# Performance work log

Hardware: AMD Instinct MI355X
Metric: run time of the kernel (lower is better)

Reference implementation:

```python
import jax, jax.numpy as jnp
import numpy as np

NC = 4        # num_components
HEADS = 24
DH = 64
D = HEADS * DH  # 1536
EPS = 1e-8


def setup_inputs() -> dict:
    key = jax.random.key(0)
    ks = jax.random.split(key, 7)
    btc, S, E = 4, 4096, 154
    w = lambda k: jax.random.normal(k, (D, D), jnp.float32) * 0.02
    return {
        "hidden_states": jax.random.normal(ks[0], (btc, S, D), jnp.float32),
        "encoder_hidden_states": jax.random.normal(ks[1], (btc, E, D), jnp.float32),
        "temperature": jnp.ones((1,), jnp.float32),
        "Wq": w(ks[2]),
        "Wk": w(ks[3]),
        "Wv": w(ks[4]),
        "Wo": w(ks[5]),
        "bo": jnp.zeros((D,), jnp.float32),
        "pad_length": 154,
    }


def reference(hidden_states, encoder_hidden_states, temperature, Wq, Wk, Wv, Wo, bo, pad_length):
    btc, S, d = hidden_states.shape          # batch*components, latent seq, hidden
    E = encoder_hidden_states.shape[1]       # encoder seq (== pad_length)
    b = btc // NC
    scale = DH ** -0.5
    residual = hidden_states

    def heads(x, L):  # [btc, L, D] -> [btc, H, L, dh]
        return x.reshape(btc, L, HEADS, DH).transpose(0, 2, 1, 3)

    q = heads(hidden_states @ Wq.T, S)
    k = heads(encoder_hidden_states @ Wk.T, E)
    v = heads(encoder_hidden_states @ Wv.T, E)

    # pad tokens are zeros projected through the same k/v weights (no bias -> zeros)
    pad_h = jnp.zeros((btc, pad_length, d), hidden_states.dtype)
    k_pad = heads(pad_h @ Wk.T, pad_length)
    v_pad = heads(pad_h @ Wv.T, pad_length)

    scores = jnp.einsum('bhsd,bhed->bhse', q, k) / (temperature[0] + EPS)
    scores_pad = jnp.einsum('bhsd,bhpd->bhsp', q, k_pad) * scale

    # cross-component softmax over dim 0
    scores = scores.reshape(NC, b, HEADS, S, E)
    scores_pad = scores_pad.reshape(NC, b, HEADS, S, pad_length)
    w = jax.nn.softmax(scores, axis=0)
    w_pad = jax.nn.softmax(scores_pad, axis=0) * (NC / pad_length) * (1.0 - w)

    weights = jnp.concatenate(
        [w.reshape(btc, HEADS, S, E), w_pad.reshape(btc, HEADS, S, pad_length)],
        axis=-1)                              # [btc, H, S, E+pad]
    v_cat = jnp.concatenate([v, v_pad], axis=2)  # [btc, H, E+pad, dh]

    out = jnp.einsum('bhse,bhed->bhsd', weights, v_cat)
    out = out.transpose(0, 2, 1, 3).reshape(btc, S, d)
    out = out @ Wo.T + bo
    return out + residual
```

## Files before the change

### kernel.cpp

```cpp
#include <hip/hip_runtime.h>

typedef __attribute__((ext_vector_type(8))) short short8;
typedef __attribute__((ext_vector_type(4))) float f32x4;
typedef __attribute__((ext_vector_type(4))) unsigned short us4;
typedef __attribute__((ext_vector_type(4))) float float4v;

#define GLB_PTR(p) ((const __attribute__((address_space(1))) void*)(p))
#define LDS_PTR(p) ((__attribute__((address_space(3))) void*)(p))

__device__ __forceinline__ unsigned short f2bf(float f) {
  unsigned int u = __float_as_uint(f);
  u += 0x7FFF + ((u >> 16) & 1);
  return (unsigned short)(u >> 16);
}

__global__ void cvt_kernel(const float* __restrict__ in, unsigned short* __restrict__ out, int n4) {
  int i = blockIdx.x * blockDim.x + threadIdx.x;
  int stride = gridDim.x * blockDim.x;
  for (; i < n4; i += stride) {
    float4v v = *(const float4v*)(in + (size_t)i * 4);
    us4 o;
    o[0] = f2bf(v[0]); o[1] = f2bf(v[1]); o[2] = f2bf(v[2]); o[3] = f2bf(v[3]);
    *(us4*)(out + (size_t)i * 4) = o;
  }
}

__global__ void cvt4_kernel(const float* __restrict__ w0, const float* __restrict__ w1,
                            const float* __restrict__ w2, const float* __restrict__ w3,
                            unsigned short* __restrict__ o0, unsigned short* __restrict__ o1,
                            unsigned short* __restrict__ o2, unsigned short* __restrict__ o3,
                            int n4) {
  const float* in = blockIdx.y == 0 ? w0 : blockIdx.y == 1 ? w1 : blockIdx.y == 2 ? w2 : w3;
  unsigned short* out = blockIdx.y == 0 ? o0 : blockIdx.y == 1 ? o1 : blockIdx.y == 2 ? o2 : o3;
  int i = blockIdx.x * blockDim.x + threadIdx.x;
  int stride = gridDim.x * blockDim.x;
  for (; i < n4; i += stride) {
    float4v v = *(const float4v*)(in + (size_t)i * 4);
    us4 o;
    o[0] = f2bf(v[0]); o[1] = f2bf(v[1]); o[2] = f2bf(v[2]); o[3] = f2bf(v[3]);
    *(us4*)(out + (size_t)i * 4) = o;
  }
}

template<int MODE>
__global__ __launch_bounds__(256, 2) void gemm_big(
    const unsigned short* __restrict__ A,
    const unsigned short* __restrict__ B,
    unsigned short* __restrict__ Cb,
    float* __restrict__ Cf,
    const float* __restrict__ bias,
    const float* __restrict__ resid) {
  constexpr int K = 1536, N = 1536, BK = 32, NKT = K / BK;
  __shared__ unsigned short As[3][256 * 32];
  __shared__ unsigned short Bs[3][128 * 32];

  const int bid = blockIdx.x;
  const int xcd = bid & 7, idx = bid >> 3;
  const int m0 = (xcd * 8 + idx / 12) * 256;
  const int n0 = (idx % 12) * 128;

  const int t = threadIdx.x;
  const int w = t >> 6, l = t & 63, lr = l & 15, lg = l >> 4;
  const int wr = w >> 1, wc = w & 1;
  const int ga = lg ^ (lr & 3);

  const int srow = t >> 2;
  const int sg = (t & 3) ^ (srow & 3);
  const unsigned short* aSrc = A + (size_t)(m0 + srow) * K + sg * 8;
  const unsigned short* bSrc = B + (size_t)(n0 + srow) * K + sg * 8;

  f32x4 acc[8][4] = {};

  auto stage = [&](int buf, int kt) {
    const int k0 = kt * BK;
    unsigned short* AsW = &As[buf][0] + w * 512;
    unsigned short* BsW = &Bs[buf][0] + w * 512;
#pragma unroll
    for (int i = 0; i < 4; ++i)
      __builtin_amdgcn_global_load_lds(GLB_PTR(aSrc + (size_t)(i * 64) * K + k0), LDS_PTR(AsW + i * 2048), 16, 0, 0);
#pragma unroll
    for (int i = 0; i < 2; ++i)
      __builtin_amdgcn_global_load_lds(GLB_PTR(bSrc + (size_t)(i * 64) * K + k0), LDS_PTR(BsW + i * 2048), 16, 0, 0);
  };

  auto loadfrags = [&](int buf, short8* af, short8* bfv) {
    const unsigned short* Asb = &As[buf][0];
    const unsigned short* Bsb = &Bs[buf][0];
#pragma unroll
    for (int i = 0; i < 8; ++i)
      af[i] = *(const short8*)(Asb + (wr * 128 + i * 16 + lr) * 32 + ga * 8);
#pragma unroll
    for (int j = 0; j < 4; ++j)
      bfv[j] = *(const short8*)(Bsb + (wc * 64 + j * 16 + lr) * 32 + ga * 8);
  };

  auto mfma_all = [&](short8* af, short8* bfv) {
#pragma unroll
    for (int i = 0; i < 8; ++i)
#pragma unroll
      for (int j = 0; j < 4; ++j)
        acc[i][j] = __builtin_amdgcn_mfma_f32_16x16x32_bf16(af[i], bfv[j], acc[i][j], 0, 0, 0);
  };

  stage(0, 0); stage(1, 1); stage(2, 2);

  int cur = 0;
  for (int kt = 0; kt < NKT - 3; ++kt) {
    asm volatile("s_waitcnt vmcnt(12)" ::: "memory");
    __builtin_amdgcn_s_barrier();
    __builtin_amdgcn_sched_barrier(0);
    short8 af[8], bfv[4];
    loadfrags(cur, af, bfv);
    asm volatile("s_waitcnt lgkmcnt(0)" ::: "memory");
    __builtin_amdgcn_sched_barrier(0);
    __builtin_amdgcn_s_barrier();
    __builtin_amdgcn_sched_barrier(0);
    stage(cur, kt + 3);
    __builtin_amdgcn_s_setprio(1);
    mfma_all(af, bfv);
    __builtin_amdgcn_s_setprio(0);
    cur = cur + 1; if (cur == 3) cur = 0;
  }
#pragma unroll
  for (int j = 0; j < 3; ++j) {
    if (j == 0)      asm volatile("s_waitcnt vmcnt(12)" ::: "memory");
    else if (j == 1) asm volatile("s_waitcnt vmcnt(6)" ::: "memory");
    else             asm volatile("s_waitcnt vmcnt(0)" ::: "memory");
    __builtin_amdgcn_s_barrier();
    __builtin_amdgcn_sched_barrier(0);
    short8 af[8], bfv[4];
    loadfrags(cur, af, bfv);
    mfma_all(af, bfv);
    cur = cur + 1; if (cur == 3) cur = 0;
  }

#pragma unroll
  for (int i = 0; i < 8; ++i) {
    const int rb = m0 + wr * 128 + i * 16 + lg * 4;
#pragma unroll
    for (int j = 0; j < 4; ++j) {
      const int col = n0 + wc * 64 + j * 16 + lr;
#pragma unroll
      for (int r = 0; r < 4; ++r) {
        size_t o = (size_t)(rb + r) * N + col;
        if (MODE == 0) Cb[o] = f2bf(acc[i][j][r]);
        else           Cf[o] = acc[i][j][r] + bias[col] + resid[o];
      }
    }
  }
}

__global__ __launch_bounds__(256) void gemm_kv(
    const unsigned short* __restrict__ A,
    const unsigned short* __restrict__ Bk,
    const unsigned short* __restrict__ Bv,
    unsigned short* __restrict__ Ck,
    unsigned short* __restrict__ Cv) {
  constexpr int K = 1536, N = 1536, Mc = 615;
  __shared__ unsigned short As[128 * 32];
  __shared__ unsigned short Bs[128 * 32];
  const unsigned short* B = blockIdx.y < 12 ? Bk : Bv;
  unsigned short* C = blockIdx.y < 12 ? Ck : Cv;
  const int m0 = blockIdx.x * 128, n0 = (blockIdx.y % 12) * 128;
  const int t = threadIdx.x;
  const int w = t >> 6, l = t & 63, lr = l & 15, lg = l >> 4;
  const int wr = w >> 1, wc = w & 1;
  const int srow = t >> 2, scol = (t & 3) * 8;

  f32x4 acc[4][4] = {};
  unsigned short* AsW = As + w * 512;
  unsigned short* BsW = Bs + w * 512;
  long ar0 = m0 + srow;       if (ar0 > Mc) ar0 = Mc;
  long ar1 = m0 + srow + 64;  if (ar1 > Mc) ar1 = Mc;

  for (int k0 = 0; k0 < K; k0 += 32) {
    __builtin_amdgcn_global_load_lds(GLB_PTR(A + ar0 * (long)K + k0 + scol), LDS_PTR(AsW),        16, 0, 0);
    __builtin_amdgcn_global_load_lds(GLB_PTR(A + ar1 * (long)K + k0 + scol), LDS_PTR(AsW + 2048), 16, 0, 0);
    __builtin_amdgcn_global_load_lds(GLB_PTR(B + (long)(n0 + srow) * K + k0 + scol),      LDS_PTR(BsW),        16, 0, 0);
    __builtin_amdgcn_global_load_lds(GLB_PTR(B + (long)(n0 + srow + 64) * K + k0 + scol), LDS_PTR(BsW + 2048), 16, 0, 0);
    __syncthreads();

    short8 af[4], bfv[4];
#pragma unroll
    for (int i = 0; i < 4; ++i) {
      af[i]  = *(const short8*)(As + (wr * 64 + i * 16 + lr) * 32 + lg * 8);
      bfv[i] = *(const short8*)(Bs + (wc * 64 + i * 16 + lr) * 32 + lg * 8);
    }
#pragma unroll
    for (int i = 0; i < 4; ++i)
#pragma unroll
      for (int j = 0; j < 4; ++j)
        acc[i][j] = __builtin_amdgcn_mfma_f32_16x16x32_bf16(af[i], bfv[j], acc[i][j], 0, 0, 0);
    __syncthreads();
  }

#pragma unroll
  for (int i = 0; i < 4; ++i) {
    int rb = m0 + wr * 64 + i * 16 + lg * 4;
#pragma unroll
    for (int j = 0; j < 4; ++j) {
      int col = n0 + wc * 64 + j * 16 + lr;
#pragma unroll
      for (int r = 0; r < 4; ++r)
        C[(long)(rb + r) * N + col] = f2bf(acc[i][j][r]);
    }
  }
}

__global__ void vtrans(const unsigned short* __restrict__ Vb, unsigned short* __restrict__ Vt) {
  int c = blockIdx.x / 24, h = blockIdx.x % 24;
  for (int idx = threadIdx.x; idx < 64 * 160; idx += blockDim.x) {
    int d = idx & 63, e = idx >> 6;
    unsigned short v = 0;
    if (e < 154) v = Vb[(long)(c * 154 + e) * 1536 + h * 64 + d];
    Vt[((long)((c * 24 + h) * 64 + d)) * 160 + e] = v;
  }
}

__global__ __launch_bounds__(256) void attn_kernel(
    const unsigned short* __restrict__ Qb,
    const unsigned short* __restrict__ Kb,
    const unsigned short* __restrict__ Vt,
    const float* __restrict__ temp,
    unsigned short* __restrict__ Ob) {
  __shared__ unsigned short P[4][4][16][160];
  const int h = blockIdx.y, sb = blockIdx.x;
  const int t = threadIdx.x, w = t >> 6, l = t & 63, lr = l & 15, lg = l >> 4;
  const int s0 = sb * 64 + w * 16;
  const float sc = 1.0f / (temp[0] + 1e-8f);

  short8 qf[4][2];
#pragma unroll
  for (int c = 0; c < 4; ++c)
#pragma unroll
    for (int kt = 0; kt < 2; ++kt)
      qf[c][kt] = *(const short8*)(Qb + (long)(c * 4096 + s0 + lr) * 1536 + h * 64 + kt * 32 + lg * 8);

  for (int et = 0; et < 10; ++et) {
    f32x4 sa[4] = {};
#pragma unroll
    for (int c = 0; c < 4; ++c)
#pragma unroll
      for (int kt = 0; kt < 2; ++kt) {
        short8 kf = *(const short8*)(Kb + (long)(c * 154 + et * 16 + lr) * 1536 + h * 64 + kt * 32 + lg * 8);
        sa[c] = __builtin_amdgcn_mfma_f32_16x16x32_bf16(kf, qf[c][kt], sa[c], 0, 0, 0);
      }
    float wv[4][4];
#pragma unroll
    for (int r = 0; r < 4; ++r) {
      float x0 = sa[0][r] * sc, x1 = sa[1][r] * sc, x2 = sa[2][r] * sc, x3 = sa[3][r] * sc;
      float m = fmaxf(fmaxf(x0, x1), fmaxf(x2, x3));
      float e0 = __expf(x0 - m), e1 = __expf(x1 - m), e2 = __expf(x2 - m), e3 = __expf(x3 - m);
      float inv = 1.0f / (e0 + e1 + e2 + e3);
      wv[0][r] = e0 * inv; wv[1][r] = e1 * inv; wv[2][r] = e2 * inv; wv[3][r] = e3 * inv;
    }
#pragma unroll
    for (int c = 0; c < 4; ++c) {
      us4 pk;
      pk[0] = f2bf(wv[c][0]); pk[1] = f2bf(wv[c][1]); pk[2] = f2bf(wv[c][2]); pk[3] = f2bf(wv[c][3]);
      *(us4*)&P[w][c][lr][et * 16 + lg * 4] = pk;
    }
  }
  __syncthreads();

  f32x4 o[4][4] = {};
#pragma unroll
  for (int c = 0; c < 4; ++c)
    for (int ks = 0; ks < 5; ++ks) {
      short8 pf = *(const short8*)&P[w][c][lr][ks * 32 + lg * 8];
#pragma unroll
      for (int nt = 0; nt < 4; ++nt) {
        short8 vf = *(const short8*)(Vt + (long)((c * 24 + h) * 64 + nt * 16 + lr) * 160 + ks * 32 + lg * 8);
        o[c][nt] = __builtin_amdgcn_mfma_f32_16x16x32_bf16(pf, vf, o[c][nt], 0, 0, 0);
      }
    }

#pragma unroll
  for (int c = 0; c < 4; ++c)
#pragma unroll
    for (int nt = 0; nt < 4; ++nt)
#pragma unroll
      for (int r = 0; r < 4; ++r)
        Ob[(long)(c * 4096 + s0 + lg * 4 + r) * 1536 + h * 64 + nt * 16 + lr] = f2bf(o[c][nt][r]);
}

extern "C" void kernel_launch(void* const* d_in, const int* in_sizes, int n_in,
                              void* d_out, int out_size, void* d_ws, size_t ws_size,
                              hipStream_t stream) {
  (void)in_sizes; (void)n_in; (void)out_size; (void)ws_size;
  const float* HS  = (const float*)d_in[0];
  const float* EHS = (const float*)d_in[1];
  const float* TMP = (const float*)d_in[2];
  const float* Wq  = (const float*)d_in[3];
  const float* Wk  = (const float*)d_in[4];
  const float* Wv  = (const float*)d_in[5];
  const float* Wo  = (const float*)d_in[6];
  const float* bo  = (const float*)d_in[7];

  char* ws = (char*)d_ws;
  size_t off = 0;
  unsigned short* HSb  = (unsigned short*)(ws + off); off += (size_t)16384 * 1536 * 2;
  unsigned short* Ob   = HSb;
  unsigned short* EHSb = (unsigned short*)(ws + off); off += (size_t)616 * 1536 * 2;
  unsigned short* Wqb  = (unsigned short*)(ws + off); off += (size_t)1536 * 1536 * 2;
  unsigned short* Wkb  = (unsigned short*)(ws + off); off += (size_t)1536 * 1536 * 2;
  unsigned short* Wvb  = (unsigned short*)(ws + off); off += (size_t)1536 * 1536 * 2;
  unsigned short* Wob  = (unsigned short*)(ws + off); off += (size_t)1536 * 1536 * 2;
  unsigned short* Kb   = (unsigned short*)(ws + off); off += (size_t)640 * 1536 * 2;
  unsigned short* Vb   = (unsigned short*)(ws + off); off += (size_t)640 * 1536 * 2;
  unsigned short* Vt   = (unsigned short*)(ws + off); off += (size_t)4 * 24 * 64 * 160 * 2;
  unsigned short* Qb   = (unsigned short*)d_out;

  cvt_kernel<<<2048, 256, 0, stream>>>(HS,  HSb,  16384 * 1536 / 4);
  cvt_kernel<<<512,  256, 0, stream>>>(EHS, EHSb, 616 * 1536 / 4);
  cvt4_kernel<<<dim3(576, 4), 256, 0, stream>>>(Wq, Wk, Wv, Wo, Wqb, Wkb, Wvb, Wob, 1536 * 1536 / 4);

  gemm_big<0><<<768, 256, 0, stream>>>(HSb, Wqb, Qb, nullptr, nullptr, nullptr);
  gemm_kv<<<dim3(5, 24), 256, 0, stream>>>(EHSb, Wkb, Wvb, Kb, Vb);

  vtrans<<<96, 256, 0, stream>>>(Vb, Vt);

  attn_kernel<<<dim3(64, 24), 256, 0, stream>>>(Qb, Kb, Vt, TMP, Ob);

  gemm_big<1><<<768, 256, 0, stream>>>(Ob, Wob, nullptr, (float*)d_out, bo, HS);
}
```

Baseline: 404.1 us.

## Double-buffer register fragments in GEMM and change LDS swizzle pattern

Restructures the GEMM main loop so LDS fragments for the next k-tile are loaded into a second register set while MFMAs run on the current one. This cuts the per-iteration barriers from two to one and overlaps LDS reads with compute. It also changes the XOR swizzle to use bits 1-2 of the row to reduce LDS bank conflicts. The cost is more registers for the doubled fragment arrays, which may lower occupancy, plus a reworked vmcnt schedule that must still match the three-stage global-to-LDS pipeline.

Result: slower. 416.6 us (+3.1%).

```diff
diff --git a/kernel.cpp b/kernel.cpp
--- a/kernel.cpp
+++ b/kernel.cpp
@@ -62,10 +62,10 @@
   const int t = threadIdx.x;
   const int w = t >> 6, l = t & 63, lr = l & 15, lg = l >> 4;
   const int wr = w >> 1, wc = w & 1;
-  const int ga = lg ^ (lr & 3);
+  const int ga = lg ^ ((lr >> 1) & 3);
 
   const int srow = t >> 2;
-  const int sg = (t & 3) ^ (srow & 3);
+  const int sg = (t & 3) ^ ((srow >> 1) & 3);
   const unsigned short* aSrc = A + (size_t)(m0 + srow) * K + sg * 8;
   const unsigned short* bSrc = B + (size_t)(n0 + srow) * K + sg * 8;
 
@@ -102,36 +102,30 @@
         acc[i][j] = __builtin_amdgcn_mfma_f32_16x16x32_bf16(af[i], bfv[j], acc[i][j], 0, 0, 0);
   };
 
+  short8 afA[8], bfA[4], afB[8], bfB[4];
+
+  auto iter = [&](int kt, short8* caf, short8* cbf, short8* naf, short8* nbf) {
+    if (kt < NKT - 1) {
+      if (kt < NKT - 2) asm volatile("s_waitcnt vmcnt(6)" ::: "memory");
+      else              asm volatile("s_waitcnt vmcnt(0)" ::: "memory");
+    }
+    asm volatile("s_waitcnt lgkmcnt(0)" ::: "memory");
+    __builtin_amdgcn_s_barrier();
+    if (kt + 3 < NKT) stage(kt % 3, kt + 3);
+    if (kt + 1 < NKT) loadfrags((kt + 1) % 3, naf, nbf);
+    __builtin_amdgcn_s_setprio(1);
+    mfma_all(caf, cbf);
+    __builtin_amdgcn_s_setprio(0);
+  };
+
   stage(0, 0); stage(1, 1); stage(2, 2);
-
-  int cur = 0;
-  for (int kt = 0; kt < NKT - 3; ++kt) {
-    asm volatile("s_waitcnt vmcnt(12)" ::: "memory");
-    __builtin_amdgcn_s_barrier();
-    __builtin_amdgcn_sched_barrier(0);
-    short8 af[8], bfv[4];
-    loadfrags(cur, af, bfv);
-    asm volatile("s_waitcnt lgkmcnt(0)" ::: "memory");
-    __builtin_amdgcn_sched_barrier(0);
-    __builtin_amdgcn_s_barrier();
-    __builtin_amdgcn_sched_barrier(0);
-    stage(cur, kt + 3);
-    __builtin_amdgcn_s_setprio(1);
-    mfma_all(af, bfv);
-    __builtin_amdgcn_s_setprio(0);
-    cur = cur + 1; if (cur == 3) cur = 0;
-  }
-#pragma unroll
-  for (int j = 0; j < 3; ++j) {
-    if (j == 0)      asm volatile("s_waitcnt vmcnt(12)" ::: "memory");
-    else if (j == 1) asm volatile("s_waitcnt vmcnt(6)" ::: "memory");
-    else             asm volatile("s_waitcnt vmcnt(0)" ::: "memory");
-    __builtin_amdgcn_s_barrier();
-    __builtin_amdgcn_sched_barrier(0);
-    short8 af[8], bfv[4];
-    loadfrags(cur, af, bfv);
-    mfma_all(af, bfv);
-    cur = cur + 1; if (cur == 3) cur = 0;
+  asm volatile("s_waitcnt vmcnt(12)" ::: "memory");
+  __builtin_amdgcn_s_barrier();
+  loadfrags(0, afA, bfA);
+
+  for (int kt = 0; kt < NKT; kt += 2) {
+    iter(kt,     afA, bfA, afB, bfB);
+    iter(kt + 1, afB, bfB, afA, bfA);
   }
 
 #pragma unroll
```

## Fuse V transpose into KV GEMM epilogue and prefetch K/V fragments in attention

Applied to the files above, without the earlier changes.

The KV projection GEMM now writes V directly in the transposed per-head layout that attention consumes, which removes the separate vtrans kernel and the intermediate Vb buffer. The attention kernel double-buffers K fragments across the QK tiles and V fragments across the PV steps, so global loads are issued ahead of the MFMAs that need them. P entries past the 154 valid encoder positions are explicitly zeroed. Vt's padded columns are no longer written by any kernel and depend on the masked P to stay harmless, while the extra live fragments raise register pressure.

Result: faster. 391.6 us (-3.1%).

```diff
diff --git a/kernel.cpp b/kernel.cpp
--- a/kernel.cpp
+++ b/kernel.cpp
@@ -155,12 +155,11 @@
     const unsigned short* __restrict__ Bk,
     const unsigned short* __restrict__ Bv,
     unsigned short* __restrict__ Ck,
-    unsigned short* __restrict__ Cv) {
+    unsigned short* __restrict__ Vt) {
   constexpr int K = 1536, N = 1536, Mc = 615;
   __shared__ unsigned short As[128 * 32];
   __shared__ unsigned short Bs[128 * 32];
   const unsigned short* B = blockIdx.y < 12 ? Bk : Bv;
-  unsigned short* C = blockIdx.y < 12 ? Ck : Cv;
   const int m0 = blockIdx.x * 128, n0 = (blockIdx.y % 12) * 128;
   const int t = threadIdx.x;
   const int w = t >> 6, l = t & 63, lr = l & 15, lg = l >> 4;
@@ -194,26 +193,37 @@
     __syncthreads();
   }
 
-#pragma unroll
-  for (int i = 0; i < 4; ++i) {
-    int rb = m0 + wr * 64 + i * 16 + lg * 4;
-#pragma unroll
-    for (int j = 0; j < 4; ++j) {
-      int col = n0 + wc * 64 + j * 16 + lr;
-#pragma unroll
-      for (int r = 0; r < 4; ++r)
-        C[(long)(rb + r) * N + col] = f2bf(acc[i][j][r]);
-    }
-  }
-}
-
-__global__ void vtrans(const unsigned short* __restrict__ Vb, unsigned short* __restrict__ Vt) {
-  int c = blockIdx.x / 24, h = blockIdx.x % 24;
-  for (int idx = threadIdx.x; idx < 64 * 160; idx += blockDim.x) {
-    int d = idx & 63, e = idx >> 6;
-    unsigned short v = 0;
-    if (e < 154) v = Vb[(long)(c * 154 + e) * 1536 + h * 64 + d];
-    Vt[((long)((c * 24 + h) * 64 + d)) * 160 + e] = v;
+  if (blockIdx.y < 12) {
+#pragma unroll
+    for (int i = 0; i < 4; ++i) {
+      int rb = m0 + wr * 64 + i * 16 + lg * 4;
+#pragma unroll
+      for (int j = 0; j < 4; ++j) {
+        int col = n0 + wc * 64 + j * 16 + lr;
+#pragma unroll
+        for (int r = 0; r < 4; ++r)
+          Ck[(long)(rb + r) * N + col] = f2bf(acc[i][j][r]);
+      }
+    }
+  } else {
+#pragma unroll
+    for (int i = 0; i < 4; ++i) {
+      int rb = m0 + wr * 64 + i * 16 + lg * 4;
+#pragma unroll
+      for (int j = 0; j < 4; ++j) {
+        int col = n0 + wc * 64 + j * 16 + lr;
+        int hh = col >> 6, dd = col & 63;
+#pragma unroll
+        for (int r = 0; r < 4; ++r) {
+          int m = rb + r;
+          if (m < 616) {
+            int c = (unsigned)m / 154u;
+            int e = m - c * 154;
+            Vt[((long)((c * 24 + hh) * 64 + dd)) * 160 + e] = f2bf(acc[i][j][r]);
+          }
+        }
+      }
+    }
   }
 }
 
@@ -236,15 +246,23 @@
     for (int kt = 0; kt < 2; ++kt)
       qf[c][kt] = *(const short8*)(Qb + (long)(c * 4096 + s0 + lr) * 1536 + h * 64 + kt * 32 + lg * 8);
 
-  for (int et = 0; et < 10; ++et) {
+  short8 kA[4][2], kB[4][2];
+  auto loadK = [&](int et, short8 (&k)[4][2]) {
+#pragma unroll
+    for (int c = 0; c < 4; ++c)
+#pragma unroll
+      for (int kt = 0; kt < 2; ++kt)
+        k[c][kt] = *(const short8*)(Kb + (long)(c * 154 + et * 16 + lr) * 1536 + h * 64 + kt * 32 + lg * 8);
+  };
+
+  auto qk_step = [&](int et, short8 (&kc)[4][2], short8 (&kn)[4][2], bool pre) {
+    if (pre) loadK(et + 1, kn);
     f32x4 sa[4] = {};
 #pragma unroll
     for (int c = 0; c < 4; ++c)
 #pragma unroll
-      for (int kt = 0; kt < 2; ++kt) {
-        short8 kf = *(const short8*)(Kb + (long)(c * 154 + et * 16 + lr) * 1536 + h * 64 + kt * 32 + lg * 8);
-        sa[c] = __builtin_amdgcn_mfma_f32_16x16x32_bf16(kf, qf[c][kt], sa[c], 0, 0, 0);
-      }
+      for (int kt = 0; kt < 2; ++kt)
+        sa[c] = __builtin_amdgcn_mfma_f32_16x16x32_bf16(kc[c][kt], qf[c][kt], sa[c], 0, 0, 0);
     float wv[4][4];
 #pragma unroll
     for (int r = 0; r < 4; ++r) {
@@ -257,23 +275,46 @@
 #pragma unroll
     for (int c = 0; c < 4; ++c) {
       us4 pk;
-      pk[0] = f2bf(wv[c][0]); pk[1] = f2bf(wv[c][1]); pk[2] = f2bf(wv[c][2]); pk[3] = f2bf(wv[c][3]);
+#pragma unroll
+      for (int r = 0; r < 4; ++r)
+        pk[r] = (et * 16 + lg * 4 + r < 154) ? f2bf(wv[c][r]) : (unsigned short)0;
       *(us4*)&P[w][c][lr][et * 16 + lg * 4] = pk;
     }
+  };
+
+  loadK(0, kA);
+#pragma unroll
+  for (int et = 0; et < 10; et += 2) {
+    qk_step(et,     kA, kB, true);
+    qk_step(et + 1, kB, kA, et + 1 < 9);
   }
   __syncthreads();
 
+  short8 vA[4], vB[4];
+  auto loadV = [&](int c, int ks, short8 (&v)[4]) {
+#pragma unroll
+    for (int nt = 0; nt < 4; ++nt)
+      v[nt] = *(const short8*)(Vt + (long)((c * 24 + h) * 64 + nt * 16 + lr) * 160 + ks * 32 + lg * 8);
+  };
+
   f32x4 o[4][4] = {};
-#pragma unroll
-  for (int c = 0; c < 4; ++c)
-    for (int ks = 0; ks < 5; ++ks) {
-      short8 pf = *(const short8*)&P[w][c][lr][ks * 32 + lg * 8];
-#pragma unroll
-      for (int nt = 0; nt < 4; ++nt) {
-        short8 vf = *(const short8*)(Vt + (long)((c * 24 + h) * 64 + nt * 16 + lr) * 160 + ks * 32 + lg * 8);
-        o[c][nt] = __builtin_amdgcn_mfma_f32_16x16x32_bf16(pf, vf, o[c][nt], 0, 0, 0);
-      }
-    }
+  loadV(0, 0, vA);
+#pragma unroll
+  for (int p = 0; p < 10; ++p) {
+    const int i0 = 2 * p, i1 = 2 * p + 1;
+    const int c0 = i0 / 5, k0 = i0 % 5;
+    const int c1 = i1 / 5, k1 = i1 % 5;
+    loadV(c1, k1, vB);
+    short8 pf0 = *(const short8*)&P[w][c0][lr][k0 * 32 + lg * 8];
+#pragma unroll
+    for (int nt = 0; nt < 4; ++nt)
+      o[c0][nt] = __builtin_amdgcn_mfma_f32_16x16x32_bf16(pf0, vA[nt], o[c0][nt], 0, 0, 0);
+    if (p < 9) loadV((i1 + 1) / 5, (i1 + 1) % 5, vA);
+    short8 pf1 = *(const short8*)&P[w][c1][lr][k1 * 32 + lg * 8];
+#pragma unroll
+    for (int nt = 0; nt < 4; ++nt)
+      o[c1][nt] = __builtin_amdgcn_mfma_f32_16x16x32_bf16(pf1, vB[nt], o[c1][nt], 0, 0, 0);
+  }
 
 #pragma unroll
   for (int c = 0; c < 4; ++c)
@@ -307,7 +348,6 @@
   unsigned short* Wvb  = (unsigned short*)(ws + off); off += (size_t)1536 * 1536 * 2;
   unsigned short* Wob  = (unsigned short*)(ws + off); off += (size_t)1536 * 1536 * 2;
   unsigned short* Kb   = (unsigned short*)(ws + off); off += (size_t)640 * 1536 * 2;
-  unsigned short* Vb   = (unsigned short*)(ws + off); off += (size_t)640 * 1536 * 2;
   unsigned short* Vt   = (unsigned short*)(ws + off); off += (size_t)4 * 24 * 64 * 160 * 2;
   unsigned short* Qb   = (unsigned short*)d_out;
 
@@ -316,9 +356,7 @@
   cvt4_kernel<<<dim3(576, 4), 256, 0, stream>>>(Wq, Wk, Wv, Wo, Wqb, Wkb, Wvb, Wob, 1536 * 1536 / 4);
 
   gemm_big<0><<<768, 256, 0, stream>>>(HSb, Wqb, Qb, nullptr, nullptr, nullptr);
-  gemm_kv<<<dim3(5, 24), 256, 0, stream>>>(EHSb, Wkb, Wvb, Kb, Vb);
-
-  vtrans<<<96, 256, 0, stream>>>(Vb, Vt);
+  gemm_kv<<<dim3(5, 24), 256, 0, stream>>>(EHSb, Wkb, Wvb, Kb, Vt);
 
   attn_kernel<<<dim3(64, 24), 256, 0, stream>>>(Qb, Kb, Vt, TMP, Ob);
 
```
